# Optimization experiments

Hardware: AMD Instinct MI355X
Metric: run time of the kernel (lower is better)

## Reference

```python
import jax, jax.numpy as jnp
import numpy as np

N = 500_000      # lidar points
ODOM = 3
ACT = 5


def setup_inputs() -> dict:
    key = jax.random.key(0)
    ks = jax.random.split(key, 40)
    f32 = jnp.float32
    def rn(k, shape, s=0.05):
        return jax.random.normal(k, shape, dtype=f32) * s
    d = {
        "x": rn(ks[0], (3 + 2 * N,), 1.0),
        "hx": rn(ks[1], (1, 128), 1.0),
        "cx": rn(ks[2], (1, 128), 1.0),
        # PointNet: conv1d k=1 == per-point matmul
        "c1w": rn(ks[3], (16, 2)),  "c1b": rn(ks[4], (16,)),
        "c2w": rn(ks[5], (32, 16)), "c2b": rn(ks[6], (32,)),
        "c3w": rn(ks[7], (64, 32)), "c3b": rn(ks[8], (64,)),
        "fcw": rn(ks[9], (64, 64)), "fcb": rn(ks[10], (64,)),
        # odom net 3->8->8
        "o1w": rn(ks[11], (8, 3)),  "o1b": rn(ks[12], (8,)),
        "o2w": rn(ks[13], (8, 8)),  "o2b": rn(ks[14], (8,)),
        # prior 72->128
        "pw": rn(ks[15], (128, 72)), "pb": rn(ks[16], (128,)),
        # LSTMCell(128,128): torch gate order i,f,g,o
        "wih": rn(ks[17], (512, 128)), "whh": rn(ks[18], (512, 128)),
        "bih": rn(ks[19], (512,)),     "bhh": rn(ks[20], (512,)),
        # post 128->64->64
        "q1w": rn(ks[21], (64, 128)), "q1b": rn(ks[22], (64,)),
        "q2w": rn(ks[23], (64, 64)),  "q2b": rn(ks[24], (64,)),
        # actor 64->16->ACT, softmax
        "aw1": rn(ks[25], (16, 64)), "ab1": rn(ks[26], (16,)),
        "aw2": rn(ks[27], (ACT, 16)), "ab2": rn(ks[28], (ACT,)),
        # critics 64->16->1
        "ciw1": rn(ks[29], (16, 64)), "cib1": rn(ks[30], (16,)),
        "ciw2": rn(ks[31], (1, 16)),  "cib2": rn(ks[32], (1,)),
        "cew1": rn(ks[33], (16, 64)), "ceb1": rn(ks[34], (16,)),
        "cew2": rn(ks[35], (1, 16)),  "ceb2": rn(ks[36], (1,)),
    }
    return d


def reference(x, hx, cx,
              c1w, c1b, c2w, c2b, c3w, c3b, fcw, fcb,
              o1w, o1b, o2w, o2b, pw, pb,
              wih, whh, bih, bhh,
              q1w, q1b, q2w, q2b,
              aw1, ab1, aw2, ab2,
              ciw1, cib1, ciw2, cib2,
              cew1, ceb1, cew2, ceb2):
    odom = x[:ODOM]                       # (3,)
    pts = x[ODOM:].reshape(2, N)          # (2, N)
    # PointNet: three 1x1 convs (per-point matmuls) + global max + fc
    h = jax.nn.relu(c1w @ pts + c1b[:, None])   # (16, N)
    h = jax.nn.relu(c2w @ h + c2b[:, None])     # (32, N)
    h = jax.nn.relu(c3w @ h + c3b[:, None])     # (64, N)
    feat = jnp.max(h, axis=1)                    # (64,)
    obs = fcw @ feat + fcb                       # (64,)
    # odom net
    pose = jax.nn.relu(o2w @ jax.nn.sigmoid(o1w @ odom + o1b) + o2b)  # (8,)
    # prior MLP
    z = jax.nn.relu(pw @ jnp.concatenate([obs, pose]) + pb)           # (128,)
    # LSTMCell (torch semantics, gate order i,f,g,o)
    gates = z @ wih.T + bih + hx[0] @ whh.T + bhh                     # (512,)
    i, f, g, o = jnp.split(gates, 4)
    c_new = jax.nn.sigmoid(f) * cx[0] + jax.nn.sigmoid(i) * jnp.tanh(g)
    h_new = jax.nn.sigmoid(o) * jnp.tanh(c_new)                       # (128,)
    hx2 = h_new[None, :]
    cx2 = c_new[None, :]
    # post MLP
    zp = jax.nn.relu(q1w @ h_new + q1b)
    zp = jax.nn.relu(q2w @ zp + q2b)                                  # (64,)
    # heads
    actor = jax.nn.softmax(aw2 @ jax.nn.relu(aw1 @ zp + ab1) + ab2)   # (ACT,)
    ci = ciw2 @ jax.nn.relu(ciw1 @ zp + cib1) + cib2                  # (1,)
    ce = cew2 @ jax.nn.relu(cew1 @ zp + ceb1) + ceb2                  # (1,)
    return (actor, ci, ce, hx2, cx2, pose)
```

## Files before the change

kernel.cpp:

```cpp
#include <hip/hip_runtime.h>

#define NBLK 1024

#define WS_Z    0
#define WS_GHH  128
#define WS_HNEW 640
#define WS_ZP1  768
#define WS_FEAT 840
#define WS_BAR  992
#define WS_PART 1024

#define NTB 16

typedef __attribute__((ext_vector_type(8))) short bf16x8;
typedef __attribute__((ext_vector_type(4))) float f32x4;

union U4 { unsigned int u[4]; bf16x8 v; };

static __device__ __forceinline__ unsigned int pack_bf16(float lo, float hi) {
    return (__float_as_uint(hi) & 0xFFFF0000u) | (__float_as_uint(lo) >> 16);
}

static __device__ __forceinline__ void ag_store(float* p, float v) {
    __hip_atomic_store(p, v, __ATOMIC_RELEASE, __HIP_MEMORY_SCOPE_AGENT);
}
static __device__ __forceinline__ float ag_load(const float* p) {
    return __hip_atomic_load(p, __ATOMIC_ACQUIRE, __HIP_MEMORY_SCOPE_AGENT);
}

static __device__ __forceinline__ void bar_sync(unsigned int* bar, int idx) {
    __syncthreads();
    if (threadIdx.x == 0) {
        __hip_atomic_fetch_add(&bar[idx], 1u, __ATOMIC_ACQ_REL, __HIP_MEMORY_SCOPE_AGENT);
        while (__hip_atomic_load(&bar[idx], __ATOMIC_ACQUIRE,
                                 __HIP_MEMORY_SCOPE_AGENT) < NTB) {}
    }
    __syncthreads();
}

__global__ __launch_bounds__(64) void prep_kernel(unsigned int* __restrict__ g)
{
    g[threadIdx.x & 63] = 0u;
}

__global__ __launch_bounds__(256) void encoder_kernel(
    const float* __restrict__ x,
    const float* __restrict__ c1w, const float* __restrict__ c1b,
    const float* __restrict__ c2w, const float* __restrict__ c2b,
    const float* __restrict__ c3w,
    float* __restrict__ ws, int N, int use_atomic)
{
    __shared__ float sW1x[16], sW1y[16], sB1s[16];
    __shared__ float sW2[512], sB2[32];
    __shared__ float sW3[2048];
    __shared__ unsigned int sh2[4 * 272];
    __shared__ float wred[4 * 64];

    int t = threadIdx.x;
    if (blockIdx.x == 0 && t < 8) ((unsigned int*)ws)[WS_BAR + t] = 0u;
    if (t < 16) { sW1x[t] = c1w[2 * t]; sW1y[t] = c1w[2 * t + 1]; sB1s[t] = c1b[t]; }
    if (t < 32) sB2[t] = c2b[t];
    for (int i = t; i < 512; i += 256)  sW2[i] = c2w[i];
    for (int i = t; i < 2048; i += 256) sW3[i] = c3w[i];
    __syncthreads();

    const int lane = t & 63, wid = t >> 6;
    const int n16 = lane & 15, q = lane >> 4;

    bf16x8 a2[2];
#pragma unroll
    for (int tt = 0; tt < 2; ++tt)
#pragma unroll
        for (int j = 0; j < 8; ++j) {
            int k = q * 8 + j;
            float w = (k < 16) ? sW2[(tt * 16 + n16) * 16 + k] : 0.0f;
            a2[tt][j] = (short)(__float_as_uint(w) >> 16);
        }
    bf16x8 a3[4];
#pragma unroll
    for (int tt = 0; tt < 4; ++tt)
#pragma unroll
        for (int j = 0; j < 8; ++j) {
            float w = sW3[(tt * 16 + n16) * 32 + q * 8 + j];
            a3[tt][j] = (short)(__float_as_uint(w) >> 16);
        }
    float w1x[8], w1y[8], b1v[8];
#pragma unroll
    for (int j = 0; j < 8; ++j) {
        int k = q * 8 + j;
        if (k < 16) { w1x[j] = sW1x[k]; w1y[j] = sW1y[k]; b1v[j] = sB1s[k]; }
        else        { w1x[j] = 0.f;     w1y[j] = 0.f;     b1v[j] = 0.f; }
    }
    float b2a[4], b2b[4];
#pragma unroll
    for (int r = 0; r < 4; ++r) { b2a[r] = sB2[q * 4 + r]; b2b[r] = sB2[16 + q * 4 + r]; }

    float vmax[16];
#pragma unroll
    for (int i = 0; i < 16; ++i) vmax[i] = -INFINITY;

    unsigned int* hb = sh2 + wid * 272;
    const int WPG = NBLK * 4;
    const int gw = blockIdx.x * 4 + wid;
    const int niter = (N + WPG * 16 - 1) / (WPG * 16);

    int p = gw * 16 + n16; if (p >= N) p = N - 1;
    float px = x[3 + p], py = x[3 + N + p];

#pragma unroll 1
    for (int it = 0; it < niter; ++it) {
        float cpx = px, cpy = py;
        if (it + 1 < niter) {
            int pn = ((it + 1) * WPG + gw) * 16 + n16;
            if (pn >= N) pn = N - 1;
            px = x[3 + pn]; py = x[3 + N + pn];
        }

        unsigned int h1d0 = 0, h1d1 = 0, h1d2 = 0, h1d3 = 0;
        if (q < 2) {
            float h0 = fmaxf(fmaf(w1x[0], cpx, fmaf(w1y[0], cpy, b1v[0])), 0.f);
            float h1 = fmaxf(fmaf(w1x[1], cpx, fmaf(w1y[1], cpy, b1v[1])), 0.f);
            float h2 = fmaxf(fmaf(w1x[2], cpx, fmaf(w1y[2], cpy, b1v[2])), 0.f);
            float h3 = fmaxf(fmaf(w1x[3], cpx, fmaf(w1y[3], cpy, b1v[3])), 0.f);
            float h4 = fmaxf(fmaf(w1x[4], cpx, fmaf(w1y[4], cpy, b1v[4])), 0.f);
            float h5 = fmaxf(fmaf(w1x[5], cpx, fmaf(w1y[5], cpy, b1v[5])), 0.f);
            float h6 = fmaxf(fmaf(w1x[6], cpx, fmaf(w1y[6], cpy, b1v[6])), 0.f);
            float h7 = fmaxf(fmaf(w1x[7], cpx, fmaf(w1y[7], cpy, b1v[7])), 0.f);
            h1d0 = pack_bf16(h0, h1); h1d1 = pack_bf16(h2, h3);
            h1d2 = pack_bf16(h4, h5); h1d3 = pack_bf16(h6, h7);
        }
        U4 bu; bu.u[0] = h1d0; bu.u[1] = h1d1; bu.u[2] = h1d2; bu.u[3] = h1d3;

        f32x4 z4 = {0.f, 0.f, 0.f, 0.f};
        f32x4 acc2a = __builtin_amdgcn_mfma_f32_16x16x32_bf16(a2[0], bu.v, z4, 0, 0, 0);
        f32x4 acc2b = __builtin_amdgcn_mfma_f32_16x16x32_bf16(a2[1], bu.v, z4, 0, 0, 0);

        unsigned int base = (unsigned int)(n16 * 17);
        hb[base + 2 * q]     = pack_bf16(fmaxf(acc2a[0] + b2a[0], 0.f),
                                         fmaxf(acc2a[1] + b2a[1], 0.f));
        hb[base + 2 * q + 1] = pack_bf16(fmaxf(acc2a[2] + b2a[2], 0.f),
                                         fmaxf(acc2a[3] + b2a[3], 0.f));
        hb[base + 8 + 2 * q] = pack_bf16(fmaxf(acc2b[0] + b2b[0], 0.f),
                                         fmaxf(acc2b[1] + b2b[1], 0.f));
        hb[base + 9 + 2 * q] = pack_bf16(fmaxf(acc2b[2] + b2b[2], 0.f),
                                         fmaxf(acc2b[3] + b2b[3], 0.f));
        __builtin_amdgcn_s_waitcnt(0xc07f);
        U4 ru;
        ru.u[0] = hb[base + 4 * q];     ru.u[1] = hb[base + 4 * q + 1];
        ru.u[2] = hb[base + 4 * q + 2]; ru.u[3] = hb[base + 4 * q + 3];

        f32x4 o0 = __builtin_amdgcn_mfma_f32_16x16x32_bf16(a3[0], ru.v, z4, 0, 0, 0);
        f32x4 o1 = __builtin_amdgcn_mfma_f32_16x16x32_bf16(a3[1], ru.v, z4, 0, 0, 0);
        f32x4 o2 = __builtin_amdgcn_mfma_f32_16x16x32_bf16(a3[2], ru.v, z4, 0, 0, 0);
        f32x4 o3 = __builtin_amdgcn_mfma_f32_16x16x32_bf16(a3[3], ru.v, z4, 0, 0, 0);
#pragma unroll
        for (int r = 0; r < 4; ++r) {
            vmax[r]      = fmaxf(vmax[r],      o0[r]);
            vmax[4 + r]  = fmaxf(vmax[4 + r],  o1[r]);
            vmax[8 + r]  = fmaxf(vmax[8 + r],  o2[r]);
            vmax[12 + r] = fmaxf(vmax[12 + r], o3[r]);
        }
    }

#pragma unroll
    for (int i = 0; i < 16; ++i) {
        float v = vmax[i];
        v = fmaxf(v, __shfl_xor(v, 1, 64));
        v = fmaxf(v, __shfl_xor(v, 2, 64));
        v = fmaxf(v, __shfl_xor(v, 4, 64));
        v = fmaxf(v, __shfl_xor(v, 8, 64));
        vmax[i] = v;
    }
    if (n16 == 0) {
#pragma unroll
        for (int tt = 0; tt < 4; ++tt)
#pragma unroll
            for (int r = 0; r < 4; ++r)
                wred[wid * 64 + tt * 16 + q * 4 + r] = vmax[tt * 4 + r];
    }
    __syncthreads();
    if (t < 64) {
        float m = fmaxf(fmaxf(wred[t], wred[64 + t]),
                        fmaxf(wred[128 + t], wred[192 + t]));
        if (use_atomic) {
            unsigned int b = __float_as_uint(m);
            unsigned int e = (b & 0x80000000u) ? ~b : (b | 0x80000000u);
            atomicMax((unsigned int*)ws + WS_PART + t, e);
        } else {
            ws[WS_PART + blockIdx.x * 64 + t] = m;
        }
    }
}

__global__ __launch_bounds__(256) void tail_fused(
    const float* __restrict__ x,   const float* __restrict__ hx,
    const float* __restrict__ cx,  const float* __restrict__ c3b,
    const float* __restrict__ fcw, const float* __restrict__ fcb,
    const float* __restrict__ o1w, const float* __restrict__ o1b,
    const float* __restrict__ o2w, const float* __restrict__ o2b,
    const float* __restrict__ pw,  const float* __restrict__ pb,
    const float* __restrict__ wih, const float* __restrict__ whh,
    const float* __restrict__ bih, const float* __restrict__ bhh,
    const float* __restrict__ q1w, const float* __restrict__ q1b,
    const float* __restrict__ q2w, const float* __restrict__ q2b,
    const float* __restrict__ aw1, const float* __restrict__ ab1,
    const float* __restrict__ aw2, const float* __restrict__ ab2,
    const float* __restrict__ ciw1, const float* __restrict__ cib1,
    const float* __restrict__ ciw2, const float* __restrict__ cib2,
    const float* __restrict__ cew1, const float* __restrict__ ceb1,
    const float* __restrict__ cew2, const float* __restrict__ ceb2,
    float* __restrict__ ws, float* __restrict__ out, int use_atomic)
{
    const int b = blockIdx.x, t = threadIdx.x;
    unsigned int* bar = (unsigned int*)ws + WS_BAR;
    __shared__ float shx[128], inL[72], zL[128], lg[32], hnL[128];
    __shared__ float featL[64], obsL[64], zp1L[64], zp2L[64];
    __shared__ float sig8L[8], odomL[3], poseL[8];
    __shared__ float a1s[16], cih[16], ceh[16], logits[5];

    if (t < 128) shx[t] = hx[t];
    __syncthreads();
    {
        const int rl = t >> 3, sub = t & 7;
        const int gr = (rl >> 3) * 128 + b * 8 + (rl & 7);
        const float4* w4 = (const float4*)(whh + (size_t)gr * 128) + sub * 4;
        float s = 0.0f;
#pragma unroll
        for (int j = 0; j < 4; j++) {
            float4 w = w4[j];
            int k = sub * 16 + 4 * j;
            s = fmaf(w.x, shx[k], fmaf(w.y, shx[k + 1],
                fmaf(w.z, shx[k + 2], fmaf(w.w, shx[k + 3], s))));
        }
        s += __shfl_xor(s, 1, 64); s += __shfl_xor(s, 2, 64); s += __shfl_xor(s, 4, 64);
        if (sub == 0) ws[WS_GHH + gr] = bhh[gr] + s;
    }
    if (!use_atomic) {
        int w = t >> 6, lane = t & 63;
        int c = b * 4 + w;
        float m = -INFINITY;
        const float* part = ws + WS_PART;
#pragma unroll 4
        for (int j = 0; j < NBLK / 64; j++)
            m = fmaxf(m, part[(lane * (NBLK / 64) + j) * 64 + c]);
#pragma unroll
        for (int off = 32; off > 0; off >>= 1)
            m = fmaxf(m, __shfl_xor(m, off, 64));
        if (lane == 0) ag_store(&ws[WS_FEAT + c], fmaxf(m + c3b[c], 0.0f));
    } else if (b == 0 && t >= 128 && t < 192) {
        int c = t - 128;
        unsigned int u = ((unsigned int*)ws)[WS_PART + c];
        unsigned int bb = (u & 0x80000000u) ? (u ^ 0x80000000u) : ~u;
        ag_store(&ws[WS_FEAT + c], fmaxf(__uint_as_float(bb) + c3b[c], 0.0f));
    }
    if (b == 0) {
        if (t < 3) odomL[t] = x[t];
        __syncthreads();
        if (t < 8) {
            float s = o1b[t];
            for (int k = 0; k < 3; k++) s = fmaf(o1w[t * 3 + k], odomL[k], s);
            sig8L[t] = 1.0f / (1.0f + expf(-s));
        }
        __syncthreads();
        if (t < 8) {
            float s = o2b[t];
            for (int k = 0; k < 8; k++) s = fmaf(o2w[t * 8 + k], sig8L[k], s);
            float pv = fmaxf(s, 0.0f);
            poseL[t] = pv;
            out[263 + t] = pv;
        }
    }
    bar_sync(bar, 0);

    if (b == 0) {
        if (t < 64) featL[t] = ag_load(&ws[WS_FEAT + t]);
        __syncthreads();
        {
            int row = t >> 2, sub = t & 3;
            const float4* f4 = (const float4*)(fcw + (size_t)row * 64) + sub * 4;
            float s = 0.0f;
#pragma unroll
            for (int j = 0; j < 4; j++) {
                float4 w = f4[j];
                int k = sub * 16 + 4 * j;
                s = fmaf(w.x, featL[k], fmaf(w.y, featL[k + 1],
                    fmaf(w.z, featL[k + 2], fmaf(w.w, featL[k + 3], s))));
            }
            s += __shfl_xor(s, 1, 64); s += __shfl_xor(s, 2, 64);
            if (sub == 0) obsL[row] = s + fcb[row];
        }
        __syncthreads();
        if (t < 64) inL[t] = obsL[t];
        else if (t < 72) inL[t] = poseL[t - 64];
        __syncthreads();
        {
            int row = t >> 1, sub = t & 1;
            const float4* p4 = (const float4*)(pw + (size_t)row * 72) + sub * 9;
            float s = 0.0f;
#pragma unroll
            for (int j = 0; j < 9; j++) {
                float4 w = p4[j];
                int k = sub * 36 + 4 * j;
                s = fmaf(w.x, inL[k], fmaf(w.y, inL[k + 1],
                    fmaf(w.z, inL[k + 2], fmaf(w.w, inL[k + 3], s))));
            }
            s += __shfl_xor(s, 1, 64);
            if (sub == 0) ag_store(&ws[WS_Z + row], fmaxf(s + pb[row], 0.0f));
        }
    }
    bar_sync(bar, 1);

    if (t < 128) zL[t] = ag_load(&ws[WS_Z + t]);
    __syncthreads();
    {
        const int rl = t >> 3, sub = t & 7;
        const int gr = (rl >> 3) * 128 + b * 8 + (rl & 7);
        const float4* w4 = (const float4*)(wih + (size_t)gr * 128) + sub * 4;
        float s = 0.0f;
#pragma unroll
        for (int j = 0; j < 4; j++) {
            float4 w = w4[j];
            int k = sub * 16 + 4 * j;
            s = fmaf(w.x, zL[k], fmaf(w.y, zL[k + 1],
                fmaf(w.z, zL[k + 2], fmaf(w.w, zL[k + 3], s))));
        }
        s += __shfl_xor(s, 1, 64); s += __shfl_xor(s, 2, 64); s += __shfl_xor(s, 4, 64);
        if (sub == 0) lg[rl] = ws[WS_GHH + gr] + bih[gr] + s;
    }
    __syncthreads();
    if (t < 8) {
        int c = b * 8 + t;
        float gI = lg[t], gF = lg[8 + t], gG = lg[16 + t], gO = lg[24 + t];
        float ig = 1.0f / (1.0f + expf(-gI));
        float fg = 1.0f / (1.0f + expf(-gF));
        float gg = tanhf(gG);
        float og = 1.0f / (1.0f + expf(-gO));
        float cn = fg * cx[c] + ig * gg;
        float hn = og * tanhf(cn);
        out[7 + c] = hn;
        out[135 + c] = cn;
        ag_store(&ws[WS_HNEW + c], hn);
    }
    bar_sync(bar, 2);

    if (t < 128) hnL[t] = ag_load(&ws[WS_HNEW + t]);
    __syncthreads();
    {
        int row = b * 4 + (t >> 6), lane = t & 63;
        const float* wr = q1w + (size_t)row * 128;
        float s = fmaf(wr[2 * lane], hnL[2 * lane], wr[2 * lane + 1] * hnL[2 * lane + 1]);
#pragma unroll
        for (int off = 32; off > 0; off >>= 1) s += __shfl_xor(s, off, 64);
        if (lane == 0) ag_store(&ws[WS_ZP1 + row], fmaxf(s + q1b[row], 0.0f));
    }
    bar_sync(bar, 3);

    if (b == 0) {
        if (t < 64) zp1L[t] = ag_load(&ws[WS_ZP1 + t]);
        __syncthreads();
        {
            int row = t >> 2, sub = t & 3;
            const float4* q4 = (const float4*)(q2w + (size_t)row * 64) + sub * 4;
            float s = 0.0f;
#pragma unroll
            for (int j = 0; j < 4; j++) {
                float4 w = q4[j];
                int k = sub * 16 + 4 * j;
                s = fmaf(w.x, zp1L[k], fmaf(w.y, zp1L[k + 1],
                    fmaf(w.z, zp1L[k + 2], fmaf(w.w, zp1L[k + 3], s))));
            }
            s += __shfl_xor(s, 1, 64); s += __shfl_xor(s, 2, 64);
            if (sub == 0) zp2L[row] = fmaxf(s + q2b[row], 0.0f);
        }
        __syncthreads();
        if (t < 16) {
            float s = ab1[t];
            for (int k = 0; k < 64; k++) s = fmaf(aw1[t * 64 + k], zp2L[k], s);
            a1s[t] = fmaxf(s, 0.0f);
        } else if (t < 32) {
            int r = t - 16;
            float s = cib1[r];
            for (int k = 0; k < 64; k++) s = fmaf(ciw1[r * 64 + k], zp2L[k], s);
            cih[r] = fmaxf(s, 0.0f);
        } else if (t < 48) {
            int r = t - 32;
            float s = ceb1[r];
            for (int k = 0; k < 64; k++) s = fmaf(cew1[r * 64 + k], zp2L[k], s);
            ceh[r] = fmaxf(s, 0.0f);
        }
        __syncthreads();
        if (t < 5) {
            float s = ab2[t];
            for (int k = 0; k < 16; k++) s = fmaf(aw2[t * 16 + k], a1s[k], s);
            logits[t] = s;
        } else if (t == 5) {
            float s = cib2[0];
            for (int k = 0; k < 16; k++) s = fmaf(ciw2[k], cih[k], s);
            out[5] = s;
        } else if (t == 6) {
            float s = ceb2[0];
            for (int k = 0; k < 16; k++) s = fmaf(cew2[k], ceh[k], s);
            out[6] = s;
        }
        __syncthreads();
        if (t == 0) {
            float m = logits[0];
            for (int i = 1; i < 5; i++) m = fmaxf(m, logits[i]);
            float e[5], s = 0.0f;
            for (int i = 0; i < 5; i++) { e[i] = expf(logits[i] - m); s += e[i]; }
            for (int i = 0; i < 5; i++) out[i] = e[i] / s;
        }
    }
}

extern "C" void kernel_launch(void* const* d_in, const int* in_sizes, int n_in,
                              void* d_out, int out_size, void* d_ws, size_t ws_size,
                              hipStream_t stream)
{
    const float* x    = (const float*)d_in[0];
    const float* hx   = (const float*)d_in[1];
    const float* cx   = (const float*)d_in[2];
    const float* c1w  = (const float*)d_in[3];
    const float* c1b  = (const float*)d_in[4];
    const float* c2w  = (const float*)d_in[5];
    const float* c2b  = (const float*)d_in[6];
    const float* c3w  = (const float*)d_in[7];
    const float* c3b  = (const float*)d_in[8];
    const float* fcw  = (const float*)d_in[9];
    const float* fcb  = (const float*)d_in[10];
    const float* o1w  = (const float*)d_in[11];
    const float* o1b  = (const float*)d_in[12];
    const float* o2w  = (const float*)d_in[13];
    const float* o2b  = (const float*)d_in[14];
    const float* pw   = (const float*)d_in[15];
    const float* pb   = (const float*)d_in[16];
    const float* wih  = (const float*)d_in[17];
    const float* whh  = (const float*)d_in[18];
    const float* bih  = (const float*)d_in[19];
    const float* bhh  = (const float*)d_in[20];
    const float* q1w  = (const float*)d_in[21];
    const float* q1b  = (const float*)d_in[22];
    const float* q2w  = (const float*)d_in[23];
    const float* q2b  = (const float*)d_in[24];
    const float* aw1  = (const float*)d_in[25];
    const float* ab1  = (const float*)d_in[26];
    const float* aw2  = (const float*)d_in[27];
    const float* ab2  = (const float*)d_in[28];
    const float* ciw1 = (const float*)d_in[29];
    const float* cib1 = (const float*)d_in[30];
    const float* ciw2 = (const float*)d_in[31];
    const float* cib2 = (const float*)d_in[32];
    const float* cew1 = (const float*)d_in[33];
    const float* ceb1 = (const float*)d_in[34];
    const float* cew2 = (const float*)d_in[35];
    const float* ceb2 = (const float*)d_in[36];

    int N = (in_sizes[0] - 3) / 2;
    size_t need = (size_t)(1024 + NBLK * 64) * 4;
    int use_atomic = (ws_size < need) ? 1 : 0;
    float* ws = (float*)d_ws;
    float* out = (float*)d_out;

    if (use_atomic)
        prep_kernel<<<1, 64, 0, stream>>>((unsigned int*)d_ws + WS_PART);
    encoder_kernel<<<NBLK, 256, 0, stream>>>(x, c1w, c1b, c2w, c2b, c3w,
                                             ws, N, use_atomic);
    tail_fused<<<NTB, 256, 0, stream>>>(x, hx, cx, c3b, fcw, fcb, o1w, o1b,
                                        o2w, o2b, pw, pb, wih, whh, bih, bhh,
                                        q1w, q1b, q2w, q2b, aw1, ab1, aw2, ab2,
                                        ciw1, cib1, ciw2, cib2, cew1, ceb1,
                                        cew2, ceb2, ws, out, use_atomic);
}
```

Before: 159.9 us.

## Process two point tiles per wave and prefetch head weights, dropping one grid barrier

The encoder now has each wave handle 32 points per iteration instead of 16. The layer-1 work that was idle in the upper lanes computes the second tile, and a lane shuffle moves it into a second MFMA operand, which halves the loop count. The head kernel prefetches the wih, fcw, pw, q1w and q2w rows into registers before the barriers, so those loads overlap the synchronisation waits. The q1 layer moves into block 0, which removes one grid-wide barrier and the WS_ZP1 round trip through global memory. The cost is higher register pressure and a larger shared buffer, plus serial q1 work on a single block.

```diff
diff --git a/kernel.cpp b/kernel.cpp
--- a/kernel.cpp
+++ b/kernel.cpp
@@ -5,7 +5,6 @@
 #define WS_Z    0
 #define WS_GHH  128
 #define WS_HNEW 640
-#define WS_ZP1  768
 #define WS_FEAT 840
 #define WS_BAR  992
 #define WS_PART 1024
@@ -53,7 +52,7 @@
     __shared__ float sW1x[16], sW1y[16], sB1s[16];
     __shared__ float sW2[512], sB2[32];
     __shared__ float sW3[2048];
-    __shared__ unsigned int sh2[4 * 272];
+    __shared__ unsigned int sh2[4 * 544];
     __shared__ float wred[4 * 64];
 
     int t = threadIdx.x;
@@ -66,6 +65,8 @@
 
     const int lane = t & 63, wid = t >> 6;
     const int n16 = lane & 15, q = lane >> 4;
+    const int g = q >> 1;
+    const int kb = (q & 1) * 8;
 
     bf16x8 a2[2];
 #pragma unroll
@@ -87,9 +88,7 @@
     float w1x[8], w1y[8], b1v[8];
 #pragma unroll
     for (int j = 0; j < 8; ++j) {
-        int k = q * 8 + j;
-        if (k < 16) { w1x[j] = sW1x[k]; w1y[j] = sW1y[k]; b1v[j] = sB1s[k]; }
-        else        { w1x[j] = 0.f;     w1y[j] = 0.f;     b1v[j] = 0.f; }
+        w1x[j] = sW1x[kb + j]; w1y[j] = sW1y[kb + j]; b1v[j] = sB1s[kb + j];
     }
     float b2a[4], b2b[4];
 #pragma unroll
@@ -99,66 +98,87 @@
 #pragma unroll
     for (int i = 0; i < 16; ++i) vmax[i] = -INFINITY;
 
-    unsigned int* hb = sh2 + wid * 272;
+    unsigned int* hbA = sh2 + wid * 544;
+    unsigned int* hbB = hbA + 272;
     const int WPG = NBLK * 4;
     const int gw = blockIdx.x * 4 + wid;
-    const int niter = (N + WPG * 16 - 1) / (WPG * 16);
-
-    int p = gw * 16 + n16; if (p >= N) p = N - 1;
+    const int niter = (N + WPG * 32 - 1) / (WPG * 32);
+
+    int p = gw * 32 + g * 16 + n16; if (p >= N) p = N - 1;
     float px = x[3 + p], py = x[3 + N + p];
 
 #pragma unroll 1
     for (int it = 0; it < niter; ++it) {
         float cpx = px, cpy = py;
         if (it + 1 < niter) {
-            int pn = ((it + 1) * WPG + gw) * 16 + n16;
+            int pn = (it + 1) * WPG * 32 + gw * 32 + g * 16 + n16;
             if (pn >= N) pn = N - 1;
             px = x[3 + pn]; py = x[3 + N + pn];
         }
 
-        unsigned int h1d0 = 0, h1d1 = 0, h1d2 = 0, h1d3 = 0;
+        float h[8];
+#pragma unroll
+        for (int j = 0; j < 8; ++j)
+            h[j] = fmaxf(fmaf(w1x[j], cpx, fmaf(w1y[j], cpy, b1v[j])), 0.f);
+        unsigned int d0 = pack_bf16(h[0], h[1]), d1 = pack_bf16(h[2], h[3]);
+        unsigned int d2 = pack_bf16(h[4], h[5]), d3 = pack_bf16(h[6], h[7]);
+        unsigned int o0 = (unsigned int)__shfl_xor((int)d0, 32, 64);
+        unsigned int o1 = (unsigned int)__shfl_xor((int)d1, 32, 64);
+        unsigned int o2 = (unsigned int)__shfl_xor((int)d2, 32, 64);
+        unsigned int o3 = (unsigned int)__shfl_xor((int)d3, 32, 64);
+        U4 buA, buB;
         if (q < 2) {
-            float h0 = fmaxf(fmaf(w1x[0], cpx, fmaf(w1y[0], cpy, b1v[0])), 0.f);
-            float h1 = fmaxf(fmaf(w1x[1], cpx, fmaf(w1y[1], cpy, b1v[1])), 0.f);
-            float h2 = fmaxf(fmaf(w1x[2], cpx, fmaf(w1y[2], cpy, b1v[2])), 0.f);
-            float h3 = fmaxf(fmaf(w1x[3], cpx, fmaf(w1y[3], cpy, b1v[3])), 0.f);
-            float h4 = fmaxf(fmaf(w1x[4], cpx, fmaf(w1y[4], cpy, b1v[4])), 0.f);
-            float h5 = fmaxf(fmaf(w1x[5], cpx, fmaf(w1y[5], cpy, b1v[5])), 0.f);
-            float h6 = fmaxf(fmaf(w1x[6], cpx, fmaf(w1y[6], cpy, b1v[6])), 0.f);
-            float h7 = fmaxf(fmaf(w1x[7], cpx, fmaf(w1y[7], cpy, b1v[7])), 0.f);
-            h1d0 = pack_bf16(h0, h1); h1d1 = pack_bf16(h2, h3);
-            h1d2 = pack_bf16(h4, h5); h1d3 = pack_bf16(h6, h7);
-        }
-        U4 bu; bu.u[0] = h1d0; bu.u[1] = h1d1; bu.u[2] = h1d2; bu.u[3] = h1d3;
+            buA.u[0] = d0; buA.u[1] = d1; buA.u[2] = d2; buA.u[3] = d3;
+            buB.u[0] = o0; buB.u[1] = o1; buB.u[2] = o2; buB.u[3] = o3;
+        } else {
+            buA.u[0] = buA.u[1] = buA.u[2] = buA.u[3] = 0u;
+            buB.u[0] = buB.u[1] = buB.u[2] = buB.u[3] = 0u;
+        }
 
         f32x4 z4 = {0.f, 0.f, 0.f, 0.f};
-        f32x4 acc2a = __builtin_amdgcn_mfma_f32_16x16x32_bf16(a2[0], bu.v, z4, 0, 0, 0);
-        f32x4 acc2b = __builtin_amdgcn_mfma_f32_16x16x32_bf16(a2[1], bu.v, z4, 0, 0, 0);
+        f32x4 aA0 = __builtin_amdgcn_mfma_f32_16x16x32_bf16(a2[0], buA.v, z4, 0, 0, 0);
+        f32x4 aA1 = __builtin_amdgcn_mfma_f32_16x16x32_bf16(a2[1], buA.v, z4, 0, 0, 0);
+        f32x4 aB0 = __builtin_amdgcn_mfma_f32_16x16x32_bf16(a2[0], buB.v, z4, 0, 0, 0);
+        f32x4 aB1 = __builtin_amdgcn_mfma_f32_16x16x32_bf16(a2[1], buB.v, z4, 0, 0, 0);
 
         unsigned int base = (unsigned int)(n16 * 17);
-        hb[base + 2 * q]     = pack_bf16(fmaxf(acc2a[0] + b2a[0], 0.f),
-                                         fmaxf(acc2a[1] + b2a[1], 0.f));
-        hb[base + 2 * q + 1] = pack_bf16(fmaxf(acc2a[2] + b2a[2], 0.f),
-                                         fmaxf(acc2a[3] + b2a[3], 0.f));
-        hb[base + 8 + 2 * q] = pack_bf16(fmaxf(acc2b[0] + b2b[0], 0.f),
-                                         fmaxf(acc2b[1] + b2b[1], 0.f));
-        hb[base + 9 + 2 * q] = pack_bf16(fmaxf(acc2b[2] + b2b[2], 0.f),
-                                         fmaxf(acc2b[3] + b2b[3], 0.f));
+        hbA[base + 2 * q]     = pack_bf16(fmaxf(aA0[0] + b2a[0], 0.f),
+                                          fmaxf(aA0[1] + b2a[1], 0.f));
+        hbA[base + 2 * q + 1] = pack_bf16(fmaxf(aA0[2] + b2a[2], 0.f),
+                                          fmaxf(aA0[3] + b2a[3], 0.f));
+        hbA[base + 8 + 2 * q] = pack_bf16(fmaxf(aA1[0] + b2b[0], 0.f),
+                                          fmaxf(aA1[1] + b2b[1], 0.f));
+        hbA[base + 9 + 2 * q] = pack_bf16(fmaxf(aA1[2] + b2b[2], 0.f),
+                                          fmaxf(aA1[3] + b2b[3], 0.f));
+        hbB[base + 2 * q]     = pack_bf16(fmaxf(aB0[0] + b2a[0], 0.f),
+                                          fmaxf(aB0[1] + b2a[1], 0.f));
+        hbB[base + 2 * q + 1] = pack_bf16(fmaxf(aB0[2] + b2a[2], 0.f),
+                                          fmaxf(aB0[3] + b2a[3], 0.f));
+        hbB[base + 8 + 2 * q] = pack_bf16(fmaxf(aB1[0] + b2b[0], 0.f),
+                                          fmaxf(aB1[1] + b2b[1], 0.f));
+        hbB[base + 9 + 2 * q] = pack_bf16(fmaxf(aB1[2] + b2b[2], 0.f),
+                                          fmaxf(aB1[3] + b2b[3], 0.f));
         __builtin_amdgcn_s_waitcnt(0xc07f);
-        U4 ru;
-        ru.u[0] = hb[base + 4 * q];     ru.u[1] = hb[base + 4 * q + 1];
-        ru.u[2] = hb[base + 4 * q + 2]; ru.u[3] = hb[base + 4 * q + 3];
-
-        f32x4 o0 = __builtin_amdgcn_mfma_f32_16x16x32_bf16(a3[0], ru.v, z4, 0, 0, 0);
-        f32x4 o1 = __builtin_amdgcn_mfma_f32_16x16x32_bf16(a3[1], ru.v, z4, 0, 0, 0);
-        f32x4 o2 = __builtin_amdgcn_mfma_f32_16x16x32_bf16(a3[2], ru.v, z4, 0, 0, 0);
-        f32x4 o3 = __builtin_amdgcn_mfma_f32_16x16x32_bf16(a3[3], ru.v, z4, 0, 0, 0);
+        U4 ruA, ruB;
+        ruA.u[0] = hbA[base + 4 * q];     ruA.u[1] = hbA[base + 4 * q + 1];
+        ruA.u[2] = hbA[base + 4 * q + 2]; ruA.u[3] = hbA[base + 4 * q + 3];
+        ruB.u[0] = hbB[base + 4 * q];     ruB.u[1] = hbB[base + 4 * q + 1];
+        ruB.u[2] = hbB[base + 4 * q + 2]; ruB.u[3] = hbB[base + 4 * q + 3];
+
+        f32x4 oA0 = __builtin_amdgcn_mfma_f32_16x16x32_bf16(a3[0], ruA.v, z4, 0, 0, 0);
+        f32x4 oA1 = __builtin_amdgcn_mfma_f32_16x16x32_bf16(a3[1], ruA.v, z4, 0, 0, 0);
+        f32x4 oA2 = __builtin_amdgcn_mfma_f32_16x16x32_bf16(a3[2], ruA.v, z4, 0, 0, 0);
+        f32x4 oA3 = __builtin_amdgcn_mfma_f32_16x16x32_bf16(a3[3], ruA.v, z4, 0, 0, 0);
+        f32x4 oB0 = __builtin_amdgcn_mfma_f32_16x16x32_bf16(a3[0], ruB.v, z4, 0, 0, 0);
+        f32x4 oB1 = __builtin_amdgcn_mfma_f32_16x16x32_bf16(a3[1], ruB.v, z4, 0, 0, 0);
+        f32x4 oB2 = __builtin_amdgcn_mfma_f32_16x16x32_bf16(a3[2], ruB.v, z4, 0, 0, 0);
+        f32x4 oB3 = __builtin_amdgcn_mfma_f32_16x16x32_bf16(a3[3], ruB.v, z4, 0, 0, 0);
 #pragma unroll
         for (int r = 0; r < 4; ++r) {
-            vmax[r]      = fmaxf(vmax[r],      o0[r]);
-            vmax[4 + r]  = fmaxf(vmax[4 + r],  o1[r]);
-            vmax[8 + r]  = fmaxf(vmax[8 + r],  o2[r]);
-            vmax[12 + r] = fmaxf(vmax[12 + r], o3[r]);
+            vmax[r]      = fmaxf(vmax[r],      fmaxf(oA0[r], oB0[r]));
+            vmax[4 + r]  = fmaxf(vmax[4 + r],  fmaxf(oA1[r], oB1[r]));
+            vmax[8 + r]  = fmaxf(vmax[8 + r],  fmaxf(oA2[r], oB2[r]));
+            vmax[12 + r] = fmaxf(vmax[12 + r], fmaxf(oA3[r], oB3[r]));
         }
     }
 
@@ -218,22 +238,35 @@
     __shared__ float sig8L[8], odomL[3], poseL[8];
     __shared__ float a1s[16], cih[16], ceh[16], logits[5];
 
+    const int rl = t >> 3, sub8 = t & 7;
+    const int gr = (rl >> 3) * 128 + b * 8 + (rl & 7);
+    const float4* wih4 = (const float4*)(wih + (size_t)gr * 128) + sub8 * 4;
+    float4 wr0 = wih4[0], wr1 = wih4[1], wr2 = wih4[2], wr3 = wih4[3];
+
+    float4 fw0, fw1, fw2, fw3;
+    float4 pv0, pv1, pv2, pv3, pv4, pv5, pv6, pv7, pv8;
+    if (b == 0) {
+        const float4* f4 = (const float4*)(fcw + (size_t)(t >> 2) * 64) + (t & 3) * 4;
+        fw0 = f4[0]; fw1 = f4[1]; fw2 = f4[2]; fw3 = f4[3];
+        const float4* p4 = (const float4*)(pw + (size_t)(t >> 1) * 72) + (t & 1) * 9;
+        pv0 = p4[0]; pv1 = p4[1]; pv2 = p4[2]; pv3 = p4[3]; pv4 = p4[4];
+        pv5 = p4[5]; pv6 = p4[6]; pv7 = p4[7]; pv8 = p4[8];
+    }
+
     if (t < 128) shx[t] = hx[t];
     __syncthreads();
     {
-        const int rl = t >> 3, sub = t & 7;
-        const int gr = (rl >> 3) * 128 + b * 8 + (rl & 7);
-        const float4* w4 = (const float4*)(whh + (size_t)gr * 128) + sub * 4;
+        const float4* w4 = (const float4*)(whh + (size_t)gr * 128) + sub8 * 4;
         float s = 0.0f;
 #pragma unroll
         for (int j = 0; j < 4; j++) {
             float4 w = w4[j];
-            int k = sub * 16 + 4 * j;
+            int k = sub8 * 16 + 4 * j;
             s = fmaf(w.x, shx[k], fmaf(w.y, shx[k + 1],
                 fmaf(w.z, shx[k + 2], fmaf(w.w, shx[k + 3], s))));
         }
         s += __shfl_xor(s, 1, 64); s += __shfl_xor(s, 2, 64); s += __shfl_xor(s, 4, 64);
-        if (sub == 0) ws[WS_GHH + gr] = bhh[gr] + s;
+        if (sub8 == 0) ws[WS_GHH + gr] = bhh[gr] + s;
     }
     if (!use_atomic) {
         int w = t >> 6, lane = t & 63;
@@ -277,15 +310,16 @@
         __syncthreads();
         {
             int row = t >> 2, sub = t & 3;
-            const float4* f4 = (const float4*)(fcw + (size_t)row * 64) + sub * 4;
-            float s = 0.0f;
-#pragma unroll
-            for (int j = 0; j < 4; j++) {
-                float4 w = f4[j];
-                int k = sub * 16 + 4 * j;
-                s = fmaf(w.x, featL[k], fmaf(w.y, featL[k + 1],
-                    fmaf(w.z, featL[k + 2], fmaf(w.w, featL[k + 3], s))));
-            }
+            int k = sub * 16;
+            float s;
+            s = fmaf(fw0.x, featL[k],      fmaf(fw0.y, featL[k + 1],
+                fmaf(fw0.z, featL[k + 2],  fmaf(fw0.w, featL[k + 3], 0.0f))));
+            s = fmaf(fw1.x, featL[k + 4],  fmaf(fw1.y, featL[k + 5],
+                fmaf(fw1.z, featL[k + 6],  fmaf(fw1.w, featL[k + 7], s))));
+            s = fmaf(fw2.x, featL[k + 8],  fmaf(fw2.y, featL[k + 9],
+                fmaf(fw2.z, featL[k + 10], fmaf(fw2.w, featL[k + 11], s))));
+            s = fmaf(fw3.x, featL[k + 12], fmaf(fw3.y, featL[k + 13],
+                fmaf(fw3.z, featL[k + 14], fmaf(fw3.w, featL[k + 15], s))));
             s += __shfl_xor(s, 1, 64); s += __shfl_xor(s, 2, 64);
             if (sub == 0) obsL[row] = s + fcb[row];
         }
@@ -295,14 +329,13 @@
         __syncthreads();
         {
             int row = t >> 1, sub = t & 1;
-            const float4* p4 = (const float4*)(pw + (size_t)row * 72) + sub * 9;
+            int k = sub * 36;
             float s = 0.0f;
+            float4 pv[9] = {pv0, pv1, pv2, pv3, pv4, pv5, pv6, pv7, pv8};
 #pragma unroll
             for (int j = 0; j < 9; j++) {
-                float4 w = p4[j];
-                int k = sub * 36 + 4 * j;
-                s = fmaf(w.x, inL[k], fmaf(w.y, inL[k + 1],
-                    fmaf(w.z, inL[k + 2], fmaf(w.w, inL[k + 3], s))));
+                s = fmaf(pv[j].x, inL[k + 4 * j],     fmaf(pv[j].y, inL[k + 4 * j + 1],
+                    fmaf(pv[j].z, inL[k + 4 * j + 2], fmaf(pv[j].w, inL[k + 4 * j + 3], s))));
             }
             s += __shfl_xor(s, 1, 64);
             if (sub == 0) ag_store(&ws[WS_Z + row], fmaxf(s + pb[row], 0.0f));
@@ -313,19 +346,18 @@
     if (t < 128) zL[t] = ag_load(&ws[WS_Z + t]);
     __syncthreads();
     {
-        const int rl = t >> 3, sub = t & 7;
-        const int gr = (rl >> 3) * 128 + b * 8 + (rl & 7);
-        const float4* w4 = (const float4*)(wih + (size_t)gr * 128) + sub * 4;
-        float s = 0.0f;
-#pragma unroll
-        for (int j = 0; j < 4; j++) {
-            float4 w = w4[j];
-            int k = sub * 16 + 4 * j;
-            s = fmaf(w.x, zL[k], fmaf(w.y, zL[k + 1],
-                fmaf(w.z, zL[k + 2], fmaf(w.w, zL[k + 3], s))));
-        }
+        int k = sub8 * 16;
+        float s;
+        s = fmaf(wr0.x, zL[k],      fmaf(wr0.y, zL[k + 1],
+            fmaf(wr0.z, zL[k + 2],  fmaf(wr0.w, zL[k + 3], 0.0f))));
+        s = fmaf(wr1.x, zL[k + 4],  fmaf(wr1.y, zL[k + 5],
+            fmaf(wr1.z, zL[k + 6],  fmaf(wr1.w, zL[k + 7], s))));
+        s = fmaf(wr2.x, zL[k + 8],  fmaf(wr2.y, zL[k + 9],
+            fmaf(wr2.z, zL[k + 10], fmaf(wr2.w, zL[k + 11], s))));
+        s = fmaf(wr3.x, zL[k + 12], fmaf(wr3.y, zL[k + 13],
+            fmaf(wr3.z, zL[k + 14], fmaf(wr3.w, zL[k + 15], s))));
         s += __shfl_xor(s, 1, 64); s += __shfl_xor(s, 2, 64); s += __shfl_xor(s, 4, 64);
-        if (sub == 0) lg[rl] = ws[WS_GHH + gr] + bih[gr] + s;
+        if (sub8 == 0) lg[rl] = ws[WS_GHH + gr] + bih[gr] + s;
     }
     __syncthreads();
     if (t < 8) {
@@ -341,33 +373,43 @@
         out[135 + c] = cn;
         ag_store(&ws[WS_HNEW + c], hn);
     }
+    float4 q1r0, q1r1, q1r2, q1r3, q1r4, q1r5, q1r6, q1r7;
+    float4 q2r0, q2r1, q2r2, q2r3;
+    if (b == 0) {
+        const float4* a4 = (const float4*)(q1w + (size_t)(t >> 2) * 128) + (t & 3) * 8;
+        q1r0 = a4[0]; q1r1 = a4[1]; q1r2 = a4[2]; q1r3 = a4[3];
+        q1r4 = a4[4]; q1r5 = a4[5]; q1r6 = a4[6]; q1r7 = a4[7];
+        const float4* b4 = (const float4*)(q2w + (size_t)(t >> 2) * 64) + (t & 3) * 4;
+        q2r0 = b4[0]; q2r1 = b4[1]; q2r2 = b4[2]; q2r3 = b4[3];
+    }
     bar_sync(bar, 2);
 
-    if (t < 128) hnL[t] = ag_load(&ws[WS_HNEW + t]);
-    __syncthreads();
-    {
-        int row = b * 4 + (t >> 6), lane = t & 63;
-        const float* wr = q1w + (size_t)row * 128;
-        float s = fmaf(wr[2 * lane], hnL[2 * lane], wr[2 * lane + 1] * hnL[2 * lane + 1]);
-#pragma unroll
-        for (int off = 32; off > 0; off >>= 1) s += __shfl_xor(s, off, 64);
-        if (lane == 0) ag_store(&ws[WS_ZP1 + row], fmaxf(s + q1b[row], 0.0f));
-    }
-    bar_sync(bar, 3);
-
     if (b == 0) {
-        if (t < 64) zp1L[t] = ag_load(&ws[WS_ZP1 + t]);
+        if (t < 128) hnL[t] = ag_load(&ws[WS_HNEW + t]);
         __syncthreads();
         {
             int row = t >> 2, sub = t & 3;
-            const float4* q4 = (const float4*)(q2w + (size_t)row * 64) + sub * 4;
+            int k = sub * 32;
+            float4 qr[8] = {q1r0, q1r1, q1r2, q1r3, q1r4, q1r5, q1r6, q1r7};
             float s = 0.0f;
 #pragma unroll
+            for (int j = 0; j < 8; j++) {
+                s = fmaf(qr[j].x, hnL[k + 4 * j],     fmaf(qr[j].y, hnL[k + 4 * j + 1],
+                    fmaf(qr[j].z, hnL[k + 4 * j + 2], fmaf(qr[j].w, hnL[k + 4 * j + 3], s))));
+            }
+            s += __shfl_xor(s, 1, 64); s += __shfl_xor(s, 2, 64);
+            if (sub == 0) zp1L[row] = fmaxf(s + q1b[row], 0.0f);
+        }
+        __syncthreads();
+        {
+            int row = t >> 2, sub = t & 3;
+            int k = sub * 16;
+            float4 qr[4] = {q2r0, q2r1, q2r2, q2r3};
+            float s = 0.0f;
+#pragma unroll
             for (int j = 0; j < 4; j++) {
-                float4 w = q4[j];
-                int k = sub * 16 + 4 * j;
-                s = fmaf(w.x, zp1L[k], fmaf(w.y, zp1L[k + 1],
-                    fmaf(w.z, zp1L[k + 2], fmaf(w.w, zp1L[k + 3], s))));
+                s = fmaf(qr[j].x, zp1L[k + 4 * j],     fmaf(qr[j].y, zp1L[k + 4 * j + 1],
+                    fmaf(qr[j].z, zp1L[k + 4 * j + 2], fmaf(qr[j].w, zp1L[k + 4 * j + 3], s))));
             }
             s += __shfl_xor(s, 1, 64); s += __shfl_xor(s, 2, 64);
             if (sub == 0) zp2L[row] = fmaxf(s + q2b[row], 0.0f);
```

Result: faster. 155.2 us (-2.9%).
